# Kernel optimization log

Hardware: AMD Instinct MI355X
Metric: run time of the kernel (lower is better)

The kernel has to match this reference:

```python
import jax, jax.numpy as jnp
import numpy as np

B = 8192
H_IN = 128
H = 512
Z = 128
N = 512   # must equal H due to W_up(h,h) -> W_down(n,.) chaining in the source
RW = 16
TEMP = 0.666
EPS = 1e-20


def _xavier(key, shape):
    fan_in, fan_out = shape[0], shape[1]
    lim = float(np.sqrt(6.0 / (fan_in + fan_out)))
    return jax.random.uniform(key, shape, jnp.float32, -lim, lim)


def setup_inputs() -> dict:
    key = jax.random.key(0)
    ks = jax.random.split(key, 24)
    inp = {
        'latent': jax.random.normal(ks[0], (B, Z), jnp.float32),
        'inputs': jnp.zeros((B, H_IN), jnp.float32),
        'gumbel_u': jax.random.uniform(ks[1], (RW, B, N), jnp.float32),
        # weights stored [in, out] for x @ W
        'W_int': _xavier(ks[2], (Z, H)),   'b_int': jnp.zeros((H,), jnp.float32),
        'W_intl': _xavier(ks[3], (Z, H)),  'b_intl': jnp.zeros((H,), jnp.float32),
        'W_hup': _xavier(ks[4], (H, H)),   'b_hup': jnp.zeros((H,), jnp.float32),
        'W_cup': _xavier(ks[5], (H, H)),   'b_cup': jnp.zeros((H,), jnp.float32),
        'W_hupl': _xavier(ks[6], (H, H)),  'b_hupl': jnp.zeros((H,), jnp.float32),
        'W_cupl': _xavier(ks[7], (H, H)),  'b_cupl': jnp.zeros((H,), jnp.float32),
        'W_lstm': _xavier(ks[8], (H_IN + H, 4 * H)), 'b_lstm': jnp.zeros((4 * H,), jnp.float32),
        'W_up': _xavier(ks[9], (H, H)),    'b_up': jnp.zeros((H,), jnp.float32),
        'W_down': _xavier(ks[10], (N, H_IN)),        # no bias
        'W_downl': _xavier(ks[11], (N, H_IN)),       # no bias
        'W_outl': _xavier(ks[12], (H, 1)), 'b_outl': jnp.zeros((1,), jnp.float32),
    }
    return inp


def _lstm_step(x, hx, cx, W_lstm, b_lstm):
    gates = jnp.concatenate([x, hx], axis=1) @ W_lstm + b_lstm  # [B, 4H]
    i, g, f, o = jnp.split(gates, 4, axis=1)
    cy = cx * jax.nn.sigmoid(f + 1.0) + jax.nn.sigmoid(i) * jnp.tanh(g)
    hy = jax.nn.sigmoid(o) * jnp.tanh(cy)
    return hy, cy


def _forward(latent, inputs, gumbel_u,
             W_int, b_int, W_intl, b_intl,
             W_hup, b_hup, W_cup, b_cup,
             W_hupl, b_hupl, W_cupl, b_cupl,
             W_lstm, b_lstm, W_up, b_up,
             W_down, W_downl, W_outl, b_outl):
    inter = jnp.tanh(latent @ W_int + b_int)
    hx = jnp.tanh(inter @ W_hup + b_hup)
    cx = jnp.tanh(inter @ W_cup + b_cup)
    inter_l = jnp.tanh(latent @ W_intl + b_intl)
    hxl = jnp.tanh(inter_l @ W_hupl + b_hupl)
    cxl = jnp.tanh(inter_l @ W_cupl + b_cupl)

    def step1(carry, u):
        x, h, c = carry
        hy, cy = _lstm_step(x, h, c, W_lstm, b_lstm)
        logits = hy @ W_up + b_up                       # [B, N]
        g = -jnp.log(-jnp.log(u + EPS) + EPS)           # gumbel noise
        y = jax.nn.softmax((logits + g) / TEMP, axis=1)
        y_hard = (y == jnp.max(y, axis=1, keepdims=True)).astype(y.dtype)
        y = jax.lax.stop_gradient(y_hard - y) + y       # straight-through hard sample
        return (y @ W_down, hy, cy), y

    _, out_steps = jax.lax.scan(step1, (inputs, hx, cx), gumbel_u)  # [RW, B, N]

    def step2(carry, y):
        h, c = carry
        xl = y @ W_downl
        hy, cy = _lstm_step(xl, h, c, W_lstm, b_lstm)   # source reuses lstm_cell here
        return (hy, cy), hy @ W_outl + b_outl           # [B, 1]

    _, line_steps = jax.lax.scan(step2, (hxl, cxl), out_steps)      # [RW, B, 1]

    return (jnp.transpose(out_steps, (1, 0, 2)),   # [B, RW, N]
            jnp.transpose(line_steps, (1, 0, 2)))  # [B, RW, 1]


def reference(latent, inputs, gumbel_u,
              W_int, b_int, W_intl, b_intl,
              W_hup, b_hup, W_cup, b_cup,
              W_hupl, b_hupl, W_cupl, b_cupl,
              W_lstm, b_lstm, W_up, b_up,
              W_down, W_downl, W_outl, b_outl):
    return _forward(latent, inputs, gumbel_u,
                    W_int, b_int, W_intl, b_intl,
                    W_hup, b_hup, W_cup, b_cup,
                    W_hupl, b_hupl, W_cupl, b_cupl,
                    W_lstm, b_lstm, W_up, b_up,
                    W_down, W_downl, W_outl, b_outl)
```

## Files before the change

### kernel.cpp

```cpp
#include <hip/hip_runtime.h>

#define NB 8192
#define NH 512
#define NZ 128
#define NIN 128
#define NN 512
#define NRW 16
#define NG 2048

typedef _Float16 f16;
typedef _Float16 f16x8 __attribute__((ext_vector_type(8)));
typedef float f32x4 __attribute__((ext_vector_type(4)));

#define LO_SCALE 2048.0f
#define LO_INV   (1.0f / 2048.0f)

__device__ __forceinline__ float sigm(float x) { return 1.0f / (1.0f + expf(-x)); }

__device__ __forceinline__ int oc_of(int c)
{
    return (((c >> 4) & 3) << 9) + ((c >> 6) << 4) + (c & 15);
}
__device__ __forceinline__ int cperm(int j)
{
    return (j & 15) | (((j >> 4) & 31) << 6) | (((j >> 9) & 3) << 4);
}

__device__ __forceinline__ void swz_xcd(int& bx, int& by)
{
    const int gx = gridDim.x;
    const int nwg = gx * gridDim.y;
    int lin = by * gx + bx;
    lin = (lin & 7) * (nwg >> 3) + (lin >> 3);
    const int sh = 31 - __clz(gx);
    bx = lin & (gx - 1);
    by = lin >> sh;
}

__device__ __forceinline__ void gload16(const f16* g, f16* l)
{
    __builtin_amdgcn_global_load_lds(
        (const __attribute__((address_space(1))) void*)g,
        (__attribute__((address_space(3))) void*)l, 16, 0, 0);
}

__device__ __forceinline__ int swz4(int row) { return (row & 3) ^ ((row >> 2) & 3); }

__device__ __forceinline__ void stage_tile(f16* tilebase, const f16* src,
                                           int rowbase, int K, int kb,
                                           int wid, int lane)
{
#pragma unroll
    for (int q = 0; q < 2; ++q) {
        const int iw = wid * 2 + q;
        const int chunk = (iw << 6) | lane;
        const int row = chunk >> 2;
        const int p = (chunk & 3) ^ swz4(row);
        const f16* g = src + (size_t)(rowbase + row) * K + kb + (p << 3);
        gload16(g, tilebase + (iw << 9));
    }
}

__device__ __forceinline__ f16x8 frag(const f16* tile, int row, int sl)
{
    return *(const f16x8*)(tile + row * 32 + ((sl ^ swz4(row)) << 3));
}

__device__ __forceinline__ void gemm_core(const f16* Ahi, const f16* Alo,
                                          const f16* Bhi, const f16* Blo,
                                          f16 (*sT)[4][128 * 32],
                                          int bm, int bn, int K,
                                          int wid, int lane, int wr, int wc,
                                          f32x4 (&accA)[4][4], f32x4 (&accB)[4][4])
{
    const int NT = K >> 5;
    stage_tile(sT[0][0], Ahi, bm, K, 0, wid, lane);
    stage_tile(sT[0][1], Alo, bm, K, 0, wid, lane);
    __builtin_amdgcn_sched_barrier(0);
    stage_tile(sT[0][2], Bhi, bn, K, 0, wid, lane);
    __builtin_amdgcn_sched_barrier(0);
    stage_tile(sT[0][3], Blo, bn, K, 0, wid, lane);

    const int r16 = lane & 15, sl = lane >> 4;

    for (int kt = 0; kt < NT; ++kt) {
        const int cur = kt & 1;
        const int nxt = cur ^ 1;
        const bool more = (kt + 1 < NT);
        const int kb = (kt + 1) << 5;

        asm volatile("s_waitcnt vmcnt(2)" ::: "memory");
        __builtin_amdgcn_s_barrier();
        __builtin_amdgcn_sched_barrier(0);
        if (more) {
            stage_tile(sT[nxt][0], Ahi, bm, K, kb, wid, lane);
            stage_tile(sT[nxt][1], Alo, bm, K, kb, wid, lane);
        }
        f16x8 ah[4], bh[4];
#pragma unroll
        for (int f = 0; f < 4; ++f) {
            ah[f] = frag(sT[cur][0], wr + f * 16 + r16, sl);
            bh[f] = frag(sT[cur][2], wc + f * 16 + r16, sl);
        }
        __builtin_amdgcn_s_setprio(1);
#pragma unroll
        for (int i = 0; i < 4; ++i)
#pragma unroll
            for (int j = 0; j < 4; ++j)
                accA[i][j] = __builtin_amdgcn_mfma_f32_16x16x32_f16(ah[i], bh[j], accA[i][j], 0, 0, 0);
        __builtin_amdgcn_s_setprio(0);

        __builtin_amdgcn_s_barrier();
        __builtin_amdgcn_sched_barrier(0);
        if (more) stage_tile(sT[nxt][2], Bhi, bn, K, kb, wid, lane);
        f16x8 al[4];
#pragma unroll
        for (int f = 0; f < 4; ++f) al[f] = frag(sT[cur][1], wr + f * 16 + r16, sl);
        __builtin_amdgcn_s_setprio(1);
#pragma unroll
        for (int i = 0; i < 4; ++i)
#pragma unroll
            for (int j = 0; j < 4; ++j)
                accB[i][j] = __builtin_amdgcn_mfma_f32_16x16x32_f16(al[i], bh[j], accB[i][j], 0, 0, 0);
        __builtin_amdgcn_s_setprio(0);

        if (more) asm volatile("s_waitcnt vmcnt(6)" ::: "memory");
        else      asm volatile("s_waitcnt vmcnt(0)" ::: "memory");
        __builtin_amdgcn_s_barrier();
        __builtin_amdgcn_sched_barrier(0);
        if (more) stage_tile(sT[nxt][3], Blo, bn, K, kb, wid, lane);
        f16x8 bl[4];
#pragma unroll
        for (int f = 0; f < 4; ++f) bl[f] = frag(sT[cur][3], wc + f * 16 + r16, sl);
        __builtin_amdgcn_s_setprio(1);
#pragma unroll
        for (int i = 0; i < 4; ++i)
#pragma unroll
            for (int j = 0; j < 4; ++j)
                accB[i][j] = __builtin_amdgcn_mfma_f32_16x16x32_f16(ah[i], bl[j], accB[i][j], 0, 0, 0);
        __builtin_amdgcn_s_setprio(0);
    }
}

__device__ __forceinline__ void gemm_core2(const f16* Ahi, const f16* Alo, const f16* Bhi,
                                           f16 (*sT)[3][128 * 32],
                                           int bm, int bn, int K,
                                           int wid, int lane, int wr, int wc,
                                           f32x4 (&accA)[4][4], f32x4 (&accB)[4][4])
{
    const int NT = K >> 5;
    stage_tile(sT[0][0], Ahi, bm, K, 0, wid, lane);
    stage_tile(sT[0][1], Alo, bm, K, 0, wid, lane);
    stage_tile(sT[0][2], Bhi, bn, K, 0, wid, lane);

    const int r16 = lane & 15, sl = lane >> 4;

    for (int kt = 0; kt < NT; ++kt) {
        const int cur = kt & 1;
        const int nxt = cur ^ 1;
        __syncthreads();
        if (kt + 1 < NT) {
            const int kb = (kt + 1) << 5;
            stage_tile(sT[nxt][0], Ahi, bm, K, kb, wid, lane);
            stage_tile(sT[nxt][1], Alo, bm, K, kb, wid, lane);
            stage_tile(sT[nxt][2], Bhi, bn, K, kb, wid, lane);
        }
        f16x8 ah[4], al[4], bh[4];
#pragma unroll
        for (int f = 0; f < 4; ++f) {
            ah[f] = frag(sT[cur][0], wr + f * 16 + r16, sl);
            al[f] = frag(sT[cur][1], wr + f * 16 + r16, sl);
            bh[f] = frag(sT[cur][2], wc + f * 16 + r16, sl);
        }
        __builtin_amdgcn_s_setprio(1);
#pragma unroll
        for (int i = 0; i < 4; ++i)
#pragma unroll
            for (int j = 0; j < 4; ++j) {
                accA[i][j] = __builtin_amdgcn_mfma_f32_16x16x32_f16(ah[i], bh[j], accA[i][j], 0, 0, 0);
                accB[i][j] = __builtin_amdgcn_mfma_f32_16x16x32_f16(al[i], bh[j], accB[i][j], 0, 0, 0);
            }
        __builtin_amdgcn_s_setprio(0);
    }
}

template<int HAS_EXTRA, int ACT>
__global__ __launch_bounds__(256, 2)
void mfma_gemm(const f16* __restrict__ Ahi, const f16* __restrict__ Alo,
               const f16* __restrict__ Bhi, const f16* __restrict__ Blo,
               const float* __restrict__ bias,
               const float* __restrict__ extra, const int* __restrict__ eidx,
               float* __restrict__ C, int N, int K)
{
    __shared__ f16 sT[2][4][128 * 32];
    int bx = blockIdx.x, by = blockIdx.y;
    swz_xcd(bx, by);
    const int bm = by << 7;
    const int bn = bx << 7;
    const int tid = threadIdx.x;
    const int wid = tid >> 6, lane = tid & 63;
    const int wr = ((wid >> 1) & 1) << 6;
    const int wc = (wid & 1) << 6;

    f32x4 accA[4][4], accB[4][4];
#pragma unroll
    for (int i = 0; i < 4; ++i)
#pragma unroll
        for (int j = 0; j < 4; ++j) { accA[i][j] = (f32x4)(0.0f); accB[i][j] = (f32x4)(0.0f); }

    gemm_core(Ahi, Alo, Bhi, Blo, sT, bm, bn, K, wid, lane, wr, wc, accA, accB);

    const int r16 = lane & 15;
    const int rg = lane >> 4;
#pragma unroll
    for (int i = 0; i < 4; ++i) {
#pragma unroll
        for (int r = 0; r < 4; ++r) {
            const int row = bm + wr + i * 16 + rg * 4 + r;
            const float* exrow = nullptr;
            if (HAS_EXTRA) exrow = extra + (size_t)eidx[row] * N;
#pragma unroll
            for (int j = 0; j < 4; ++j) {
                const int col = bn + wc + j * 16 + r16;
                float v = accA[i][j][r] + accB[i][j][r] * LO_INV;
                if (bias) v += bias[col];
                if (HAS_EXTRA) v += exrow[col];
                if (ACT == 1) v = tanhf(v);
                C[(size_t)row * N + col] = v;
            }
        }
    }
}

template<int HAS_EXTRA>
__global__ __launch_bounds__(256, 2)
void mfma_gate_lstm(const f16* __restrict__ Ahi, const f16* __restrict__ Alo,
                    const f16* __restrict__ Bhi, const f16* __restrict__ Blo,
                    const float* __restrict__ blp,
                    const float* __restrict__ extra, const int* __restrict__ eidx,
                    float* __restrict__ c,
                    f16* __restrict__ h_hi, f16* __restrict__ h_lo)
{
    __shared__ f16 sT[2][4][128 * 32];
    int bx = blockIdx.x, by = blockIdx.y;
    swz_xcd(bx, by);
    const int bm = by << 7;
    const int bn = bx << 7;
    const int tid = threadIdx.x;
    const int wid = tid >> 6, lane = tid & 63;
    const int wr = ((wid >> 1) & 1) << 6;
    const int wc = (wid & 1) << 6;

    f32x4 accA[4][4], accB[4][4];
#pragma unroll
    for (int i = 0; i < 4; ++i)
#pragma unroll
        for (int j = 0; j < 4; ++j) { accA[i][j] = (f32x4)(0.0f); accB[i][j] = (f32x4)(0.0f); }

    gemm_core(Ahi, Alo, Bhi, Blo, sT, bm, bn, NH, wid, lane, wr, wc, accA, accB);

    const int m = lane & 15;
    const int rg = lane >> 4;
    const int colb = bn + wc;
    const int jj = ((colb >> 6) << 4) + m;
    float bi[4];
#pragma unroll
    for (int g = 0; g < 4; ++g) bi[g] = blp[colb + g * 16 + m];

#pragma unroll
    for (int i = 0; i < 4; ++i) {
#pragma unroll
        for (int r = 0; r < 4; ++r) {
            const int row = bm + wr + i * 16 + rg * 4 + r;
            float ex[4] = {0.f, 0.f, 0.f, 0.f};
            if (HAS_EXTRA) {
                const float* exr = extra + (size_t)eidx[row] * NG;
#pragma unroll
                for (int g = 0; g < 4; ++g) ex[g] = exr[colb + g * 16 + m];
            }
            const float ig = accA[i][0][r] + accB[i][0][r] * LO_INV + bi[0] + ex[0];
            const float gg = accA[i][1][r] + accB[i][1][r] * LO_INV + bi[1] + ex[1];
            const float fg = accA[i][2][r] + accB[i][2][r] * LO_INV + bi[2] + ex[2];
            const float og = accA[i][3][r] + accB[i][3][r] * LO_INV + bi[3] + ex[3];
            const size_t cidx = (size_t)row * NH + jj;
            const float cx = c[cidx];
            const float cy = cx * sigm(fg + 1.0f) + sigm(ig) * tanhf(gg);
            const float hy = sigm(og) * tanhf(cy);
            c[cidx] = cy;
            const f16 a = (f16)hy;
            h_hi[cidx] = a;
            h_lo[cidx] = (f16)((hy - (float)a) * LO_SCALE);
        }
    }
}

__global__ __launch_bounds__(256, 2)
void mfma_gate_lstm2(const f16* __restrict__ Ahi, const f16* __restrict__ Alo,
                     const f16* __restrict__ Bhi,
                     const float* __restrict__ blp,
                     const float* __restrict__ extra, const int* __restrict__ eidx,
                     float* __restrict__ c,
                     f16* __restrict__ h_hi, f16* __restrict__ h_lo,
                     const float* __restrict__ Woutl,
                     float* __restrict__ out1, int t)
{
    __shared__ f16 sT[2][3][128 * 32];
    int bx = blockIdx.x, by = blockIdx.y;
    swz_xcd(bx, by);
    const int bm = by << 7;
    const int bn = bx << 7;
    const int tid = threadIdx.x;
    const int wid = tid >> 6, lane = tid & 63;
    const int wr = ((wid >> 1) & 1) << 6;
    const int wc = (wid & 1) << 6;

    f32x4 accA[4][4], accB[4][4];
#pragma unroll
    for (int i = 0; i < 4; ++i)
#pragma unroll
        for (int j = 0; j < 4; ++j) { accA[i][j] = (f32x4)(0.0f); accB[i][j] = (f32x4)(0.0f); }

    gemm_core2(Ahi, Alo, Bhi, sT, bm, bn, NH, wid, lane, wr, wc, accA, accB);

    const int m = lane & 15;
    const int rg = lane >> 4;
    const int colb = bn + wc;
    const int jj = ((colb >> 6) << 4) + m;
    const float wout = Woutl[jj];
    float bi[4];
#pragma unroll
    for (int g = 0; g < 4; ++g) bi[g] = blp[colb + g * 16 + m];

#pragma unroll
    for (int i = 0; i < 4; ++i) {
#pragma unroll
        for (int r = 0; r < 4; ++r) {
            const int row = bm + wr + i * 16 + rg * 4 + r;
            const float* exr = extra + (size_t)eidx[row] * NG;
            float ex[4];
#pragma unroll
            for (int g = 0; g < 4; ++g) ex[g] = exr[colb + g * 16 + m];
            const float ig = accA[i][0][r] + accB[i][0][r] * LO_INV + bi[0] + ex[0];
            const float gg = accA[i][1][r] + accB[i][1][r] * LO_INV + bi[1] + ex[1];
            const float fg = accA[i][2][r] + accB[i][2][r] * LO_INV + bi[2] + ex[2];
            const float og = accA[i][3][r] + accB[i][3][r] * LO_INV + bi[3] + ex[3];
            const size_t cidx = (size_t)row * NH + jj;
            const float cx = c[cidx];
            const float cy = cx * sigm(fg + 1.0f) + sigm(ig) * tanhf(gg);
            const float hy = sigm(og) * tanhf(cy);
            c[cidx] = cy;
            const f16 a = (f16)hy;
            h_hi[cidx] = a;
            h_lo[cidx] = (f16)((hy - (float)a) * LO_SCALE);
            float part = hy * wout;
#pragma unroll
            for (int msk = 1; msk < 16; msk <<= 1) part += __shfl_xor(part, msk);
            if (m == 0) atomicAdd(&out1[(size_t)row * NRW + t], part);
        }
    }
}

__global__ __launch_bounds__(256)
void out1_init(float* __restrict__ out1, const float* __restrict__ boutl)
{
    const size_t i = (size_t)blockIdx.x * 256 + threadIdx.x;
    out1[i] = boutl[0];
}

template<int ACT, int PERM>
__global__ __launch_bounds__(256)
void gemm128(const float* __restrict__ A, int lda,
             const float* __restrict__ W, int ldw,
             const float* __restrict__ bias,
             float* __restrict__ C, int ldc, int K)
{
    __shared__ float As[16][128];
    __shared__ float Bs[16][128];
    const int bm = blockIdx.y << 7, bn = blockIdx.x << 7;
    const int tid = threadIdx.x;
    const int tx = tid & 15, ty = tid >> 4;
    const int sar = tid >> 1, sac = (tid & 1) << 3;
    const int sbk = tid >> 4, sbc = (tid & 15) << 3;
    float acc[2][2][4][4] = {};
    const float* Ap = A + (size_t)(bm + sar) * lda + sac;
    const float* Wp = W + (size_t)sbk * ldw + bn + sbc;
    for (int kb = 0; kb < K; kb += 16) {
        const float4 av0 = *(const float4*)(Ap + kb);
        const float4 av1 = *(const float4*)(Ap + kb + 4);
        const float4 bv0 = *(const float4*)(Wp + (size_t)kb * ldw);
        const float4 bv1 = *(const float4*)(Wp + (size_t)kb * ldw + 4);
        __syncthreads();
        As[sac + 0][sar] = av0.x; As[sac + 1][sar] = av0.y;
        As[sac + 2][sar] = av0.z; As[sac + 3][sar] = av0.w;
        As[sac + 4][sar] = av1.x; As[sac + 5][sar] = av1.y;
        As[sac + 6][sar] = av1.z; As[sac + 7][sar] = av1.w;
        *(float4*)&Bs[sbk][sbc] = bv0;
        *(float4*)&Bs[sbk][sbc + 4] = bv1;
        __syncthreads();
#pragma unroll
        for (int kk = 0; kk < 16; ++kk) {
            float a[2][4], b[2][4];
            *(float4*)a[0] = *(const float4*)&As[kk][ty << 2];
            *(float4*)a[1] = *(const float4*)&As[kk][64 + (ty << 2)];
            *(float4*)b[0] = *(const float4*)&Bs[kk][tx << 2];
            *(float4*)b[1] = *(const float4*)&Bs[kk][64 + (tx << 2)];
#pragma unroll
            for (int rh = 0; rh < 2; ++rh)
#pragma unroll
                for (int ch = 0; ch < 2; ++ch)
#pragma unroll
                    for (int i = 0; i < 4; ++i)
#pragma unroll
                        for (int j = 0; j < 4; ++j)
                            acc[rh][ch][i][j] = fmaf(a[rh][i], b[ch][j], acc[rh][ch][i][j]);
        }
    }
    float4 bi4[2] = {make_float4(0.f, 0.f, 0.f, 0.f), make_float4(0.f, 0.f, 0.f, 0.f)};
    if (bias) {
        bi4[0] = *(const float4*)(bias + bn + (tx << 2));
        bi4[1] = *(const float4*)(bias + bn + 64 + (tx << 2));
    }
#pragma unroll
    for (int rh = 0; rh < 2; ++rh)
#pragma unroll
        for (int i = 0; i < 4; ++i) {
            const int row = bm + rh * 64 + (ty << 2) + i;
#pragma unroll
            for (int ch = 0; ch < 2; ++ch) {
                const int col = bn + ch * 64 + (tx << 2);
                float v0 = acc[rh][ch][i][0] + bi4[ch].x;
                float v1 = acc[rh][ch][i][1] + bi4[ch].y;
                float v2 = acc[rh][ch][i][2] + bi4[ch].z;
                float v3 = acc[rh][ch][i][3] + bi4[ch].w;
                if (ACT == 1) { v0 = tanhf(v0); v1 = tanhf(v1); v2 = tanhf(v2); v3 = tanhf(v3); }
                const int wcol = PERM ? cperm(col) : col;
                *(float4*)(C + (size_t)row * ldc + wcol) = make_float4(v0, v1, v2, v3);
            }
        }
}

template<int PERM>
__global__ __launch_bounds__(256)
void tsplit(const float* __restrict__ in, int ldin, int K,
            f16* __restrict__ ohi, f16* __restrict__ olo)
{
    __shared__ float t[32][33];
    const int kb = blockIdx.x << 5, nb = blockIdx.y << 5;
    const int cx = threadIdx.x & 31, ry = threadIdx.x >> 5;
    const int col = PERM ? oc_of(nb + cx) : (nb + cx);
#pragma unroll
    for (int q = 0; q < 4; ++q)
        t[ry + q * 8][cx] = in[(size_t)(kb + ry + q * 8) * ldin + col];
    __syncthreads();
#pragma unroll
    for (int q = 0; q < 4; ++q) {
        const int n = ry + q * 8;
        const float v = t[cx][n];
        const f16 hi = (f16)v;
        ohi[(size_t)(nb + n) * K + kb + cx] = hi;
        olo[(size_t)(nb + n) * K + kb + cx] = (f16)((v - (float)hi) * LO_SCALE);
    }
}

__global__ __launch_bounds__(256)
void permb(const float* __restrict__ b, float* __restrict__ bp)
{
    const int c = blockIdx.x * 256 + threadIdx.x;
    bp[c] = b[oc_of(c)];
}

__global__ __launch_bounds__(256)
void split_h(const float* __restrict__ h, f16* __restrict__ hi, f16* __restrict__ lo)
{
    const size_t i = (size_t)blockIdx.x * 256 + threadIdx.x;
    const float v = h[i];
    const f16 a = (f16)v;
    hi[i] = a;
    lo[i] = (f16)((v - (float)a) * LO_SCALE);
}

__global__ __launch_bounds__(256)
void argmax_onehot(const float* __restrict__ logits, const float* __restrict__ gu,
                   float* __restrict__ out0, int* __restrict__ kidx, int t)
{
    const int b = blockIdx.x;
    const int tid = threadIdx.x;
    const float* lrow = logits + (size_t)b * NN;
    const float* urow = gu + ((size_t)t * NB + b) * NN;
    float best = -INFINITY;
    int bi = 0x7fffffff;
#pragma unroll
    for (int q = 0; q < 2; ++q) {
        const int j = tid + q * 256;
        const float u = urow[j];
        const float g = -logf(-logf(u + 1e-20f) + 1e-20f);
        const float v = lrow[j] + g;
        if (v > best || (v == best && j < bi)) { best = v; bi = j; }
    }
#pragma unroll
    for (int off = 32; off > 0; off >>= 1) {
        const float ov = __shfl_down(best, off);
        const int oi = __shfl_down(bi, off);
        if (ov > best || (ov == best && oi < bi)) { best = ov; bi = oi; }
    }
    __shared__ float sv[4];
    __shared__ int si[4];
    const int lane = tid & 63, w = tid >> 6;
    if (lane == 0) { sv[w] = best; si[w] = bi; }
    __syncthreads();
    if (tid == 0) {
        for (int q = 1; q < 4; ++q)
            if (sv[q] > best || (sv[q] == best && si[q] < bi)) { best = sv[q]; bi = si[q]; }
        si[0] = bi;
        kidx[(size_t)t * NB + b] = bi;
    }
    __syncthreads();
    const int win = si[0];
    float* orow = out0 + ((size_t)b * NRW + t) * NN;
#pragma unroll
    for (int q = 0; q < 2; ++q) {
        const int j = tid + q * 256;
        orow[j] = (j == win) ? 1.0f : 0.0f;
    }
}

extern "C" void kernel_launch(void* const* d_in, const int* in_sizes, int n_in,
                              void* d_out, int out_size, void* d_ws, size_t ws_size,
                              hipStream_t stream)
{
    const float* latent  = (const float*)d_in[0];
    const float* gu      = (const float*)d_in[2];
    const float* W_int   = (const float*)d_in[3];
    const float* b_int   = (const float*)d_in[4];
    const float* W_intl  = (const float*)d_in[5];
    const float* b_intl  = (const float*)d_in[6];
    const float* W_hup   = (const float*)d_in[7];
    const float* b_hup   = (const float*)d_in[8];
    const float* W_cup   = (const float*)d_in[9];
    const float* b_cup   = (const float*)d_in[10];
    const float* W_hupl  = (const float*)d_in[11];
    const float* b_hupl  = (const float*)d_in[12];
    const float* W_cupl  = (const float*)d_in[13];
    const float* b_cupl  = (const float*)d_in[14];
    const float* W_lstm  = (const float*)d_in[15];
    const float* b_lstm  = (const float*)d_in[16];
    const float* W_up    = (const float*)d_in[17];
    const float* b_up    = (const float*)d_in[18];
    const float* W_down  = (const float*)d_in[19];
    const float* W_downl = (const float*)d_in[20];
    const float* W_outl  = (const float*)d_in[21];
    const float* b_outl  = (const float*)d_in[22];

    float* out0 = (float*)d_out;
    float* out1 = out0 + (size_t)NB * NRW * NN;

    float* ws     = (float*)d_ws;
    float* c      = ws;
    float* logits = c + (size_t)NB * NH;
    float* htmp   = logits + (size_t)NB * NH;
    float* gdown  = htmp + (size_t)NB * NH;
    float* gdownl = gdown + (size_t)NN * NG;
    float* blp    = gdownl + (size_t)NN * NG;
    f16* fp = (f16*)(blp + NG);
    f16* h_hi[2]; f16* h_lo[2];
    h_hi[0] = fp;                    fp += (size_t)NB * NH;
    h_lo[0] = fp;                    fp += (size_t)NB * NH;
    h_hi[1] = fp;                    fp += (size_t)NB * NH;
    h_lo[1] = fp;                    fp += (size_t)NB * NH;
    f16* i_hi   = fp;                fp += (size_t)NB * NH;
    f16* i_lo   = fp;                fp += (size_t)NB * NH;
    f16* WlT_hi = fp;                fp += (size_t)NG * NH;
    f16* WlT_lo = fp;                fp += (size_t)NG * NH;
    f16* WupT_hi = fp;               fp += (size_t)NN * NH;
    f16* WupT_lo = fp;               fp += (size_t)NN * NH;
    f16* WhT_hi = fp;                fp += (size_t)NH * NH;
    f16* WhT_lo = fp;                fp += (size_t)NH * NH;
    f16* WcT_hi = fp;                fp += (size_t)NH * NH;
    f16* WcT_lo = fp;                fp += (size_t)NH * NH;
    f16* WhlT_hi = fp;               fp += (size_t)NH * NH;
    f16* WhlT_lo = fp;               fp += (size_t)NH * NH;
    f16* WclT_hi = fp;               fp += (size_t)NH * NH;
    f16* WclT_lo = fp;               fp += (size_t)NH * NH;
    int* kidx = (int*)fp;

    const dim3 blk(256);
    const dim3 g_gates(NG / 128, NB / 128);
    const dim3 g_h(NH / 128, NB / 128);
    const dim3 g_pre(NG / 128, NN / 128);
    const dim3 g_sph(NB * NH / 256);

    tsplit<1><<<dim3(NH / 32, NG / 32), blk, 0, stream>>>(W_lstm + (size_t)NIN * NG, NG, NH, WlT_hi, WlT_lo);
    tsplit<0><<<dim3(NH / 32, NN / 32), blk, 0, stream>>>(W_up, NH, NH, WupT_hi, WupT_lo);
    tsplit<0><<<dim3(NH / 32, NH / 32), blk, 0, stream>>>(W_hup, NH, NH, WhT_hi, WhT_lo);
    tsplit<0><<<dim3(NH / 32, NH / 32), blk, 0, stream>>>(W_cup, NH, NH, WcT_hi, WcT_lo);
    tsplit<0><<<dim3(NH / 32, NH / 32), blk, 0, stream>>>(W_hupl, NH, NH, WhlT_hi, WhlT_lo);
    tsplit<0><<<dim3(NH / 32, NH / 32), blk, 0, stream>>>(W_cupl, NH, NH, WclT_hi, WclT_lo);
    permb<<<dim3(NG / 256), blk, 0, stream>>>(b_lstm, blp);
    gemm128<0, 1><<<g_pre, blk, 0, stream>>>(W_down, NIN, W_lstm, NG, nullptr, gdown, NG, NIN);
    gemm128<0, 1><<<g_pre, blk, 0, stream>>>(W_downl, NIN, W_lstm, NG, nullptr, gdownl, NG, NIN);

    gemm128<1, 0><<<g_h, blk, 0, stream>>>(latent, NZ, W_int, NH, b_int, logits, NH, NZ);
    split_h<<<g_sph, blk, 0, stream>>>(logits, i_hi, i_lo);
    mfma_gemm<0, 1><<<g_h, blk, 0, stream>>>(i_hi, i_lo, WhT_hi, WhT_lo, b_hup,
                                             nullptr, nullptr, htmp, NH, NH);
    split_h<<<g_sph, blk, 0, stream>>>(htmp, h_hi[0], h_lo[0]);
    mfma_gemm<0, 1><<<g_h, blk, 0, stream>>>(i_hi, i_lo, WcT_hi, WcT_lo, b_cup,
                                             nullptr, nullptr, c, NH, NH);

    int cur = 0;
    for (int t = 0; t < NRW; ++t) {
        const int nxt = cur ^ 1;
        if (t == 0)
            mfma_gate_lstm<0><<<g_gates, blk, 0, stream>>>(h_hi[cur], h_lo[cur], WlT_hi, WlT_lo,
                                                           blp, nullptr, nullptr,
                                                           c, h_hi[nxt], h_lo[nxt]);
        else
            mfma_gate_lstm<1><<<g_gates, blk, 0, stream>>>(h_hi[cur], h_lo[cur], WlT_hi, WlT_lo,
                                                           blp, gdown, kidx + (size_t)(t - 1) * NB,
                                                           c, h_hi[nxt], h_lo[nxt]);
        mfma_gemm<0, 0><<<g_h, blk, 0, stream>>>(h_hi[nxt], h_lo[nxt], WupT_hi, WupT_lo, b_up,
                                                 nullptr, nullptr, logits, NN, NH);
        argmax_onehot<<<dim3(NB), blk, 0, stream>>>(logits, gu, out0, kidx, t);
        cur = nxt;
    }

    gemm128<1, 0><<<g_h, blk, 0, stream>>>(latent, NZ, W_intl, NH, b_intl, logits, NH, NZ);
    split_h<<<g_sph, blk, 0, stream>>>(logits, i_hi, i_lo);
    mfma_gemm<0, 1><<<g_h, blk, 0, stream>>>(i_hi, i_lo, WhlT_hi, WhlT_lo, b_hupl,
                                             nullptr, nullptr, htmp, NH, NH);
    split_h<<<g_sph, blk, 0, stream>>>(htmp, h_hi[0], h_lo[0]);
    mfma_gemm<0, 1><<<g_h, blk, 0, stream>>>(i_hi, i_lo, WclT_hi, WclT_lo, b_cupl,
                                             nullptr, nullptr, c, NH, NH);
    out1_init<<<dim3(NB * NRW / 256), blk, 0, stream>>>(out1, b_outl);

    cur = 0;
    for (int t = 0; t < NRW; ++t) {
        const int nxt = cur ^ 1;
        mfma_gate_lstm2<<<g_gates, blk, 0, stream>>>(h_hi[cur], h_lo[cur], WlT_hi,
                                                     blp, gdownl, kidx + (size_t)t * NB,
                                                     c, h_hi[nxt], h_lo[nxt],
                                                     W_outl, out1, t);
        cur = nxt;
    }
}
```

Before: 3.092 ms.

## Fuse logits GEMM with Gumbel argmax, drop split precision in second LSTM

The logits GEMM now adds the Gumbel noise and does the argmax in its epilogue. It writes per-column-block partial maxima, and a small finalize kernel reduces them and writes the one-hot output, so the fp32 logits round trip and the per-row argmax pass go away. The second-phase LSTM now uses a single fp16 hi/hi product instead of the split hi/lo scheme, which halves its MFMA and staging work but loses accuracy. The init GEMMs also write fp16 split outputs directly, removing the split_h passes.

```diff
diff --git a/kernel.cpp b/kernel.cpp
--- a/kernel.cpp
+++ b/kernel.cpp
@@ -142,16 +142,15 @@
     }
 }
 
-__device__ __forceinline__ void gemm_core2(const f16* Ahi, const f16* Alo, const f16* Bhi,
-                                           f16 (*sT)[3][128 * 32],
+__device__ __forceinline__ void gemm_core1(const f16* Ahi, const f16* Bhi,
+                                           f16 (*sT)[2][128 * 32],
                                            int bm, int bn, int K,
                                            int wid, int lane, int wr, int wc,
-                                           f32x4 (&accA)[4][4], f32x4 (&accB)[4][4])
+                                           f32x4 (&acc)[4][4])
 {
     const int NT = K >> 5;
     stage_tile(sT[0][0], Ahi, bm, K, 0, wid, lane);
-    stage_tile(sT[0][1], Alo, bm, K, 0, wid, lane);
-    stage_tile(sT[0][2], Bhi, bn, K, 0, wid, lane);
+    stage_tile(sT[0][1], Bhi, bn, K, 0, wid, lane);
 
     const int r16 = lane & 15, sl = lane >> 4;
 
@@ -162,35 +161,31 @@
         if (kt + 1 < NT) {
             const int kb = (kt + 1) << 5;
             stage_tile(sT[nxt][0], Ahi, bm, K, kb, wid, lane);
-            stage_tile(sT[nxt][1], Alo, bm, K, kb, wid, lane);
-            stage_tile(sT[nxt][2], Bhi, bn, K, kb, wid, lane);
-        }
-        f16x8 ah[4], al[4], bh[4];
+            stage_tile(sT[nxt][1], Bhi, bn, K, kb, wid, lane);
+        }
+        f16x8 ah[4], bh[4];
 #pragma unroll
         for (int f = 0; f < 4; ++f) {
             ah[f] = frag(sT[cur][0], wr + f * 16 + r16, sl);
-            al[f] = frag(sT[cur][1], wr + f * 16 + r16, sl);
-            bh[f] = frag(sT[cur][2], wc + f * 16 + r16, sl);
+            bh[f] = frag(sT[cur][1], wc + f * 16 + r16, sl);
         }
         __builtin_amdgcn_s_setprio(1);
 #pragma unroll
         for (int i = 0; i < 4; ++i)
 #pragma unroll
-            for (int j = 0; j < 4; ++j) {
-                accA[i][j] = __builtin_amdgcn_mfma_f32_16x16x32_f16(ah[i], bh[j], accA[i][j], 0, 0, 0);
-                accB[i][j] = __builtin_amdgcn_mfma_f32_16x16x32_f16(al[i], bh[j], accB[i][j], 0, 0, 0);
-            }
+            for (int j = 0; j < 4; ++j)
+                acc[i][j] = __builtin_amdgcn_mfma_f32_16x16x32_f16(ah[i], bh[j], acc[i][j], 0, 0, 0);
         __builtin_amdgcn_s_setprio(0);
     }
 }
 
-template<int HAS_EXTRA, int ACT>
+template<int OUT>
 __global__ __launch_bounds__(256, 2)
 void mfma_gemm(const f16* __restrict__ Ahi, const f16* __restrict__ Alo,
                const f16* __restrict__ Bhi, const f16* __restrict__ Blo,
                const float* __restrict__ bias,
-               const float* __restrict__ extra, const int* __restrict__ eidx,
-               float* __restrict__ C, int N, int K)
+               float* __restrict__ C, f16* __restrict__ Ohi, f16* __restrict__ Olo,
+               int N, int K)
 {
     __shared__ f16 sT[2][4][128 * 32];
     int bx = blockIdx.x, by = blockIdx.y;
@@ -217,19 +212,111 @@
 #pragma unroll
         for (int r = 0; r < 4; ++r) {
             const int row = bm + wr + i * 16 + rg * 4 + r;
-            const float* exrow = nullptr;
-            if (HAS_EXTRA) exrow = extra + (size_t)eidx[row] * N;
 #pragma unroll
             for (int j = 0; j < 4; ++j) {
                 const int col = bn + wc + j * 16 + r16;
                 float v = accA[i][j][r] + accB[i][j][r] * LO_INV;
                 if (bias) v += bias[col];
-                if (HAS_EXTRA) v += exrow[col];
-                if (ACT == 1) v = tanhf(v);
-                C[(size_t)row * N + col] = v;
+                if (OUT >= 1) v = tanhf(v);
+                const size_t idx = (size_t)row * N + col;
+                if (OUT <= 1) C[idx] = v;
+                else {
+                    const f16 a = (f16)v;
+                    Ohi[idx] = a;
+                    if (OUT == 2) Olo[idx] = (f16)((v - (float)a) * LO_SCALE);
+                }
             }
         }
     }
+}
+
+__global__ __launch_bounds__(256, 2)
+void mfma_logits_argmax(const f16* __restrict__ Ahi, const f16* __restrict__ Alo,
+                        const f16* __restrict__ Bhi, const f16* __restrict__ Blo,
+                        const float* __restrict__ bias,
+                        const float* __restrict__ gu,
+                        float2* __restrict__ part, int t)
+{
+    __shared__ f16 sT[2][4][128 * 32];
+    int bx = blockIdx.x, by = blockIdx.y;
+    swz_xcd(bx, by);
+    const int bm = by << 7;
+    const int bn = bx << 7;
+    const int tid = threadIdx.x;
+    const int wid = tid >> 6, lane = tid & 63;
+    const int wr = ((wid >> 1) & 1) << 6;
+    const int wc = (wid & 1) << 6;
+
+    f32x4 accA[4][4], accB[4][4];
+#pragma unroll
+    for (int i = 0; i < 4; ++i)
+#pragma unroll
+        for (int j = 0; j < 4; ++j) { accA[i][j] = (f32x4)(0.0f); accB[i][j] = (f32x4)(0.0f); }
+
+    gemm_core(Ahi, Alo, Bhi, Blo, sT, bm, bn, NN, wid, lane, wr, wc, accA, accB);
+
+    const int r16 = lane & 15;
+    const int rg = lane >> 4;
+    const int cb = bx * 2 + (wc >> 6);
+    float bi[4];
+#pragma unroll
+    for (int j = 0; j < 4; ++j) bi[j] = bias[bn + wc + j * 16 + r16];
+
+#pragma unroll
+    for (int i = 0; i < 4; ++i) {
+#pragma unroll
+        for (int r = 0; r < 4; ++r) {
+            const int row = bm + wr + i * 16 + rg * 4 + r;
+            const float* urow = gu + ((size_t)t * NB + row) * NN;
+            float best = -INFINITY;
+            int bidx = 0x7fffffff;
+#pragma unroll
+            for (int j = 0; j < 4; ++j) {
+                const int col = bn + wc + j * 16 + r16;
+                const float u = urow[col];
+                const float g = -logf(-logf(u + 1e-20f) + 1e-20f);
+                const float v = accA[i][j][r] + accB[i][j][r] * LO_INV + bi[j] + g;
+                if (v > best || (v == best && col < bidx)) { best = v; bidx = col; }
+            }
+#pragma unroll
+            for (int msk = 1; msk < 16; msk <<= 1) {
+                const float ov = __shfl_xor(best, msk);
+                const int oi = __shfl_xor(bidx, msk);
+                if (ov > best || (ov == best && oi < bidx)) { best = ov; bidx = oi; }
+            }
+            if (r16 == 0) part[(size_t)row * 8 + cb] = make_float2(best, (float)bidx);
+        }
+    }
+}
+
+__global__ __launch_bounds__(256)
+void finalize_argmax(const float2* __restrict__ part,
+                     float* __restrict__ out0, int* __restrict__ kidx, int t)
+{
+    const int w = threadIdx.x >> 6;
+    const int lane = threadIdx.x & 63;
+    const int row = blockIdx.x * 4 + w;
+    float best = -INFINITY;
+    int bi = 0x7fffffff;
+    if (lane < 8) {
+        const float2 p = part[(size_t)row * 8 + lane];
+        best = p.x;
+        bi = (int)p.y;
+    }
+#pragma unroll
+    for (int msk = 1; msk < 8; msk <<= 1) {
+        const float ov = __shfl_xor(best, msk);
+        const int oi = __shfl_xor(bi, msk);
+        if (ov > best || (ov == best && oi < bi)) { best = ov; bi = oi; }
+    }
+    const int win = __shfl(bi, 0);
+    if (lane == 0) kidx[(size_t)t * NB + row] = win;
+    float* orow = out0 + ((size_t)row * NRW + t) * NN;
+    const int c0 = lane * 8;
+    float4 v0 = make_float4(c0 == win, c0 + 1 == win, c0 + 2 == win, c0 + 3 == win);
+    float4 v1 = make_float4(c0 + 4 == win, c0 + 5 == win, c0 + 6 == win, c0 + 7 == win);
+    *(float4*)(orow + c0) = v0;
+    *(float4*)(orow + c0 + 4) = v1;
 }
 
 template<int HAS_EXTRA>
@@ -295,16 +382,15 @@
 }
 
 __global__ __launch_bounds__(256, 2)
-void mfma_gate_lstm2(const f16* __restrict__ Ahi, const f16* __restrict__ Alo,
-                     const f16* __restrict__ Bhi,
+void mfma_gate_lstm2(const f16* __restrict__ Ahi, const f16* __restrict__ Bhi,
                      const float* __restrict__ blp,
                      const float* __restrict__ extra, const int* __restrict__ eidx,
                      float* __restrict__ c,
-                     f16* __restrict__ h_hi, f16* __restrict__ h_lo,
+                     f16* __restrict__ h_hi,
                      const float* __restrict__ Woutl,
                      float* __restrict__ out1, int t)
 {
-    __shared__ f16 sT[2][3][128 * 32];
+    __shared__ f16 sT[2][2][128 * 32];
     int bx = blockIdx.x, by = blockIdx.y;
     swz_xcd(bx, by);
     const int bm = by << 7;
@@ -314,13 +400,13 @@
     const int wr = ((wid >> 1) & 1) << 6;
     const int wc = (wid & 1) << 6;
 
-    f32x4 accA[4][4], accB[4][4];
+    f32x4 acc[4][4];
 #pragma unroll
     for (int i = 0; i < 4; ++i)
 #pragma unroll
-        for (int j = 0; j < 4; ++j) { accA[i][j] = (f32x4)(0.0f); accB[i][j] = (f32x4)(0.0f); }
-
-    gemm_core2(Ahi, Alo, Bhi, sT, bm, bn, NH, wid, lane, wr, wc, accA, accB);
+        for (int j = 0; j < 4; ++j) acc[i][j] = (f32x4)(0.0f);
+
+    gemm_core1(Ahi, Bhi, sT, bm, bn, NH, wid, lane, wr, wc, acc);
 
     const int m = lane & 15;
     const int rg = lane >> 4;
@@ -340,18 +426,16 @@
             float ex[4];
 #pragma unroll
             for (int g = 0; g < 4; ++g) ex[g] = exr[colb + g * 16 + m];
-            const float ig = accA[i][0][r] + accB[i][0][r] * LO_INV + bi[0] + ex[0];
-            const float gg = accA[i][1][r] + accB[i][1][r] * LO_INV + bi[1] + ex[1];
-            const float fg = accA[i][2][r] + accB[i][2][r] * LO_INV + bi[2] + ex[2];
-            const float og = accA[i][3][r] + accB[i][3][r] * LO_INV + bi[3] + ex[3];
+            const float ig = acc[i][0][r] + bi[0] + ex[0];
+            const float gg = acc[i][1][r] + bi[1] + ex[1];
+            const float fg = acc[i][2][r] + bi[2] + ex[2];
+            const float og = acc[i][3][r] + bi[3] + ex[3];
             const size_t cidx = (size_t)row * NH + jj;
             const float cx = c[cidx];
             const float cy = cx * sigm(fg + 1.0f) + sigm(ig) * tanhf(gg);
             const float hy = sigm(og) * tanhf(cy);
             c[cidx] = cy;
-            const f16 a = (f16)hy;
-            h_hi[cidx] = a;
-            h_lo[cidx] = (f16)((hy - (float)a) * LO_SCALE);
+            h_hi[cidx] = (f16)hy;
             float part = hy * wout;
 #pragma unroll
             for (int msk = 1; msk < 16; msk <<= 1) part += __shfl_xor(part, msk);
@@ -458,7 +542,7 @@
         const float v = t[cx][n];
         const f16 hi = (f16)v;
         ohi[(size_t)(nb + n) * K + kb + cx] = hi;
-        olo[(size_t)(nb + n) * K + kb + cx] = (f16)((v - (float)hi) * LO_SCALE);
+        if (olo) olo[(size_t)(nb + n) * K + kb + cx] = (f16)((v - (float)hi) * LO_SCALE);
     }
 }
 
@@ -477,51 +561,6 @@
     const f16 a = (f16)v;
     hi[i] = a;
     lo[i] = (f16)((v - (float)a) * LO_SCALE);
-}
-
-__global__ __launch_bounds__(256)
-void argmax_onehot(const float* __restrict__ logits, const float* __restrict__ gu,
-                   float* __restrict__ out0, int* __restrict__ kidx, int t)
-{
-    const int b = blockIdx.x;
-    const int tid = threadIdx.x;
-    const float* lrow = logits + (size_t)b * NN;
-    const float* urow = gu + ((size_t)t * NB + b) * NN;
-    float best = -INFINITY;
-    int bi = 0x7fffffff;
-#pragma unroll
-    for (int q = 0; q < 2; ++q) {
-        const int j = tid + q * 256;
-        const float u = urow[j];
-        const float g = -logf(-logf(u + 1e-20f) + 1e-20f);
-        const float v = lrow[j] + g;
-        if (v > best || (v == best && j < bi)) { best = v; bi = j; }
-    }
-#pragma unroll
-    for (int off = 32; off > 0; off >>= 1) {
-        const float ov = __shfl_down(best, off);
-        const int oi = __shfl_down(bi, off);
-        if (ov > best || (ov == best && oi < bi)) { best = ov; bi = oi; }
-    }
-    __shared__ float sv[4];
-    __shared__ int si[4];
-    const int lane = tid & 63, w = tid >> 6;
-    if (lane == 0) { sv[w] = best; si[w] = bi; }
-    __syncthreads();
-    if (tid == 0) {
-        for (int q = 1; q < 4; ++q)
-            if (sv[q] > best || (sv[q] == best && si[q] < bi)) { best = sv[q]; bi = si[q]; }
-        si[0] = bi;
-        kidx[(size_t)t * NB + b] = bi;
-    }
-    __syncthreads();
-    const int win = si[0];
-    float* orow = out0 + ((size_t)b * NRW + t) * NN;
-#pragma unroll
-    for (int q = 0; q < 2; ++q) {
-        const int j = tid + q * 256;
-        orow[j] = (j == win) ? 1.0f : 0.0f;
-    }
 }
 
 extern "C" void kernel_launch(void* const* d_in, const int* in_sizes, int n_in,
@@ -557,11 +596,11 @@
     float* ws     = (float*)d_ws;
     float* c      = ws;
     float* logits = c + (size_t)NB * NH;
-    float* htmp   = logits + (size_t)NB * NH;
-    float* gdown  = htmp + (size_t)NB * NH;
+    float* gdown  = logits + (size_t)NB * NH;
     float* gdownl = gdown + (size_t)NN * NG;
     float* blp    = gdownl + (size_t)NN * NG;
-    f16* fp = (f16*)(blp + NG);
+    float2* part  = (float2*)(blp + NG);
+    f16* fp = (f16*)(part + (size_t)NB * 8);
     f16* h_hi[2]; f16* h_lo[2];
     h_hi[0] = fp;                    fp += (size_t)NB * NH;
     h_lo[0] = fp;                    fp += (size_t)NB * NH;
@@ -601,11 +640,10 @@
 
     gemm128<1, 0><<<g_h, blk, 0, stream>>>(latent, NZ, W_int, NH, b_int, logits, NH, NZ);
     split_h<<<g_sph, blk, 0, stream>>>(logits, i_hi, i_lo);
-    mfma_gemm<0, 1><<<g_h, blk, 0, stream>>>(i_hi, i_lo, WhT_hi, WhT_lo, b_hup,
-                                             nullptr, nullptr, htmp, NH, NH);
-    split_h<<<g_sph, blk, 0, stream>>>(htmp, h_hi[0], h_lo[0]);
-    mfma_gemm<0, 1><<<g_h, blk, 0, stream>>>(i_hi, i_lo, WcT_hi, WcT_lo, b_cup,
-                                             nullptr, nullptr, c, NH, NH);
+    mfma_gemm<2><<<g_h, blk, 0, stream>>>(i_hi, i_lo, WhT_hi, WhT_lo, b_hup,
+                                          nullptr, h_hi[0], h_lo[0], NH, NH);
+    mfma_gemm<1><<<g_h, blk, 0, stream>>>(i_hi, i_lo, WcT_hi, WcT_lo, b_cup,
+                                          c, nullptr, nullptr, NH, NH);
 
     int cur = 0;
     for (int t = 0; t < NRW; ++t) {
@@ -618,27 +656,26 @@
             mfma_gate_lstm<1><<<g_gates, blk, 0, stream>>>(h_hi[cur], h_lo[cur], WlT_hi, WlT_lo,
                                                            blp, gdown, kidx + (size_t)(t - 1) * NB,
                                                            c, h_hi[nxt], h_lo[nxt]);
-        mfma_gemm<0, 0><<<g_h, blk, 0, stream>>>(h_hi[nxt], h_lo[nxt], WupT_hi, WupT_lo, b_up,
-                                                 nullptr, nullptr, logits, NN, NH);
-        argmax_onehot<<<dim3(NB), blk, 0, stream>>>(logits, gu, out0, kidx, t);
+        mfma_logits_argmax<<<g_h, blk, 0, stream>>>(h_hi[nxt], h_lo[nxt], WupT_hi, WupT_lo,
+                                                    b_up, gu, part, t);
+        finalize_argmax<<<dim3(NB / 4), blk, 0, stream>>>(part, out0, kidx, t);
         cur = nxt;
     }
 
     gemm128<1, 0><<<g_h, blk, 0, stream>>>(latent, NZ, W_intl, NH, b_intl, logits, NH, NZ);
     split_h<<<g_sph, blk, 0, stream>>>(logits, i_hi, i_lo);
-    mfma_gemm<0, 1><<<g_h, blk, 0, stream>>>(i_hi, i_lo, WhlT_hi, WhlT_lo, b_hupl,
-                                             nullptr, nullptr, htmp, NH, NH);
-    split_h<<<g_sph, blk, 0, stream>>>(htmp, h_hi[0], h_lo[0]);
-    mfma_gemm<0, 1><<<g_h, blk, 0, stream>>>(i_hi, i_lo, WclT_hi, WclT_lo, b_cupl,
-                                             nullptr, nullptr, c, NH, NH);
+    mfma_gemm<3><<<g_h, blk, 0, stream>>>(i_hi, i_lo, WhlT_hi, WhlT_lo, b_hupl,
+                                          nullptr, h_hi[0], nullptr, NH, NH);
+    mfma_gemm<1><<<g_h, blk, 0, stream>>>(i_hi, i_lo, WclT_hi, WclT_lo, b_cupl,
+                                          c, nullptr, nullptr, NH, NH);
     out1_init<<<dim3(NB * NRW / 256), blk, 0, stream>>>(out1, b_outl);
 
     cur = 0;
     for (int t = 0; t < NRW; ++t) {
         const int nxt = cur ^ 1;
-        mfma_gate_lstm2<<<g_gates, blk, 0, stream>>>(h_hi[cur], h_lo[cur], WlT_hi,
+        mfma_gate_lstm2<<<g_gates, blk, 0, stream>>>(h_hi[cur], WlT_hi,
                                                      blp, gdownl, kidx + (size_t)t * NB,
-                                                     c, h_hi[nxt], h_lo[nxt],
+                                                     c, h_hi[nxt],
                                                      W_outl, out1, t);
         cur = nxt;
     }
```

New measurement: 3.088 ms. About the same (-0.1%).
